# Kernel tuning notes

Hardware: AMD Instinct MI355X
Metric: run time of the kernel (lower is better)

Reference implementation:

```python
import jax, jax.numpy as jnp
import numpy as np

NHEAD = 8

def setup_inputs() -> dict:
    key = jax.random.key(0)
    ks = jax.random.split(key, 7)
    B, N, D = 8, 1024, 512
    scale = 1.0 / np.sqrt(D)
    return {
        "x": jax.random.normal(ks[0], (B, N, D), dtype=jnp.float32),
        "graph_bias": jax.random.normal(ks[1], (B, N, N), dtype=jnp.float32),
        "in_proj_w": jax.random.normal(ks[2], (3 * D, D), dtype=jnp.float32) * scale,
        "in_proj_b": jax.random.normal(ks[3], (3 * D,), dtype=jnp.float32) * 0.02,
        "out_proj_w": jax.random.normal(ks[4], (D, D), dtype=jnp.float32) * scale,
        "out_proj_b": jax.random.normal(ks[5], (D,), dtype=jnp.float32) * 0.02,
        "bias_strength": jnp.ones((), dtype=jnp.float32),
    }

def reference(x, graph_bias, in_proj_w, in_proj_b, out_proj_w, out_proj_b, bias_strength):
    B, N, D = x.shape
    H = NHEAD
    hd = D // H
    # fused QKV projection (matches nn.MultiheadAttention in_proj)
    qkv = x @ in_proj_w.T + in_proj_b          # (B, N, 3D)
    q, k, v = jnp.split(qkv, 3, axis=-1)
    # (B, H, N, hd)
    q = q.reshape(B, N, H, hd).transpose(0, 2, 1, 3)
    k = k.reshape(B, N, H, hd).transpose(0, 2, 1, 3)
    v = v.reshape(B, N, H, hd).transpose(0, 2, 1, 3)
    # additive bias from predicted causal structure
    alpha = jax.nn.sigmoid(bias_strength)
    causal_mask = jax.nn.sigmoid(graph_bias).transpose(0, 2, 1)   # (B, N, N)
    causal_mask = alpha * causal_mask + (1.0 - alpha) * 0.5
    attn_bias = (causal_mask - 0.5) * 10.0                        # (B, N, N)
    scores = jnp.einsum("bhqd,bhkd->bhqk", q, k) / jnp.sqrt(jnp.asarray(hd, x.dtype))
    scores = scores + attn_bias[:, None, :, :]                    # broadcast over heads
    probs = jax.nn.softmax(scores, axis=-1)
    out = jnp.einsum("bhqk,bhkd->bhqd", probs, v)                 # (B, H, N, hd)
    out = out.transpose(0, 2, 1, 3).reshape(B, N, D)
    return out @ out_proj_w.T + out_proj_b
```

## Files before the change

kernel.cpp:

```cpp
#include <hip/hip_runtime.h>

typedef __attribute__((ext_vector_type(8))) __bf16 bf16x8;
typedef __attribute__((ext_vector_type(4))) __bf16 bf16x4;
typedef __attribute__((ext_vector_type(4))) float f32x4;
typedef __attribute__((ext_vector_type(8))) _Float16 f16x8;

#define LOG2E 1.44269504088896340736f

__device__ __forceinline__ void async_load16(const void* g, void* l) {
  __builtin_amdgcn_global_load_lds(
      (const __attribute__((address_space(1))) void*)g,
      (__attribute__((address_space(3))) void*)l, 16, 0, 0);
}

__device__ __forceinline__ float fast_exp2(float x) {
#if __has_builtin(__builtin_amdgcn_exp2f)
  return __builtin_amdgcn_exp2f(x);
#else
  return __expf(x * 0.6931471805599453f);
#endif
}

__global__ void cvtW(const float* __restrict__ b, __bf16* __restrict__ ob, int nb4,
                     const float* __restrict__ c, __bf16* __restrict__ oc, int nc4) {
  int i = blockIdx.x * blockDim.x + threadIdx.x;
  int n = nb4 + nc4;
  int stride = gridDim.x * blockDim.x;
  for (; i < n; i += stride) {
    const float4* s;
    bf16x4* d;
    int j;
    if (i < nb4) { s = (const float4*)b; d = (bf16x4*)ob; j = i; }
    else { s = (const float4*)c; d = (bf16x4*)oc; j = i - nb4; }
    float4 v = s[j];
    bf16x4 o;
    o[0] = (__bf16)v.x; o[1] = (__bf16)v.y; o[2] = (__bf16)v.z; o[3] = (__bf16)v.w;
    d[j] = o;
  }
}

__global__ __launch_bounds__(512, 4) void gemm1_ebias(
    const float* __restrict__ X,
    const __bf16* __restrict__ Bm,
    const float* __restrict__ bias,
    __bf16* __restrict__ qkO,
    __bf16* __restrict__ vT,
    const float* __restrict__ gbias, const float* __restrict__ bstr,
    _Float16* __restrict__ ebT) {
  __shared__ __align__(16) char smem[32768];
  const int t = threadIdx.x;

  if (blockIdx.x >= 768) {
    const int gid = (blockIdx.x - 768) * 512 + t;
    const int lane = gid & 63;
    const int kt = (gid >> 6) & 31;
    const int qt = (gid >> 11) & 63;
    const int b = gid >> 17;
    const int g = lane >> 4, ln = lane & 15;
    const float alpha = 1.f / (1.f + __expf(-bstr[0]));
    const float bsc = 10.f * alpha * LOG2E;
    const float* base = gbias + (size_t)(b * 1024 + kt * 32 + ln) * 1024 + qt * 16 + g * 4;
    float4 va = *(const float4*)(base);
    float4 vb = *(const float4*)(base + 16 * 1024);
    float sv[8] = {va.x, va.y, va.z, va.w, vb.x, vb.y, vb.z, vb.w};
    f16x8 o;
#pragma unroll
    for (int i = 0; i < 8; ++i)
      o[i] = (_Float16)((1.f / (1.f + __expf(-sv[i])) - 0.5f) * bsc);
    *(f16x8*)(ebT + (size_t)gid * 8) = o;
    return;
  }

  char* lA = smem;
  char* lB = smem + 16384;
  const int lane = t & 63;
  const int wid = t >> 6;
  const int wm = wid >> 2, wn = wid & 3;
  const int g = lane >> 4, ln = lane & 15;
  const int wg = (blockIdx.x & 7) * 96 + (blockIdx.x >> 3);
  const int m0 = (wg / 12) * 128;
  const int n0 = (wg % 12) * 128;

  const int srow = t >> 3;
  const int sswz = ((t & 7) * 16) ^ ((srow & 7) << 4);
  const int eswz = ((t & 7) * 8) ^ ((srow & 7) << 3);
  const char* gB = (const char*)Bm + (size_t)n0 * 1024;
  const float* gX = X + (size_t)m0 * 512;

  f32x4 acc[4][2] = {};

  for (int k0 = 0; k0 < 512; k0 += 64) {
    __syncthreads();
#pragma unroll
    for (int c = 0; c < 2; ++c) {
      int row = srow + 64 * c;
      async_load16(gB + (size_t)row * 1024 + k0 * 2 + sswz, lB + c * 8192 + t * 16);
      const float* src = gX + (size_t)row * 512 + k0 + eswz;
      float4 a0 = *(const float4*)(src);
      float4 a1 = *(const float4*)(src + 4);
      bf16x8 o;
      o[0] = (__bf16)a0.x; o[1] = (__bf16)a0.y; o[2] = (__bf16)a0.z; o[3] = (__bf16)a0.w;
      o[4] = (__bf16)a1.x; o[5] = (__bf16)a1.y; o[6] = (__bf16)a1.z; o[7] = (__bf16)a1.w;
      *(bf16x8*)(lA + c * 8192 + t * 16) = o;
    }
    __syncthreads();
#pragma unroll
    for (int ks = 0; ks < 2; ++ks) {
      bf16x8 af[4], bf[2];
#pragma unroll
      for (int i = 0; i < 4; ++i) {
        int ar = wm * 64 + i * 16 + ln;
        af[i] = *(const bf16x8*)(lA + ar * 128 + ((ks * 64 + g * 16) ^ ((ar & 7) << 4)));
      }
#pragma unroll
      for (int j = 0; j < 2; ++j) {
        int br = wn * 32 + j * 16 + ln;
        bf[j] = *(const bf16x8*)(lB + br * 128 + ((ks * 64 + g * 16) ^ ((br & 7) << 4)));
      }
#pragma unroll
      for (int i = 0; i < 4; ++i)
#pragma unroll
        for (int j = 0; j < 2; ++j)
          acc[i][j] = __builtin_amdgcn_mfma_f32_16x16x32_bf16(af[i], bf[j], acc[i][j], 0, 0, 0);
    }
  }

#pragma unroll
  for (int j = 0; j < 2; ++j) {
    int col = n0 + wn * 32 + j * 16 + ln;
    float bv = bias[col];
    if (col < 1024) {
      float scale = (col < 512) ? (0.125f * LOG2E) : 1.0f;
#pragma unroll
      for (int i = 0; i < 4; ++i) {
        int row0 = m0 + wm * 64 + i * 16 + g * 4;
#pragma unroll
        for (int r = 0; r < 4; ++r)
          qkO[(size_t)(row0 + r) * 1024 + col] = (__bf16)((acc[i][j][r] + bv) * scale);
      }
    } else {
      int h = (col - 1024) >> 6;
      int d = (col - 1024) & 63;
#pragma unroll
      for (int i = 0; i < 4; ++i) {
        int row0 = m0 + wm * 64 + i * 16 + g * 4;
        int b = row0 >> 10;
        bf16x4 pk;
#pragma unroll
        for (int r = 0; r < 4; ++r) pk[r] = (__bf16)(acc[i][j][r] + bv);
        *(bf16x4*)(vT + (((size_t)b * 8 + h) * 64 + d) * 1024 + (row0 & 1023)) = pk;
      }
    }
  }
}

__global__ __launch_bounds__(512, 4) void gemm_bt0(
    const __bf16* __restrict__ A, const __bf16* __restrict__ Bm,
    const float* __restrict__ bias, float* __restrict__ C0,
    int M, int N, int K, int nt) {
  __shared__ __align__(16) char smem[32768];
  char* lA = smem;
  char* lB = smem + 16384;
  const int t = threadIdx.x;
  const int lane = t & 63;
  const int wid = t >> 6;
  const int wm = wid >> 2, wn = wid & 3;
  const int g = lane >> 4, ln = lane & 15;
  const int qchunk = gridDim.x >> 3;
  const int wg = (blockIdx.x & 7) * qchunk + (blockIdx.x >> 3);
  const int m0 = (wg / nt) * 128;
  const int n0 = (wg % nt) * 128;

  const int srow = t >> 3;
  const int sswz = ((t & 7) * 16) ^ ((srow & 7) << 4);
  const size_t KB = (size_t)K * 2;
  const char* gA = (const char*)A + (size_t)m0 * KB;
  const char* gB = (const char*)Bm + (size_t)n0 * KB;

  f32x4 acc[4][2] = {};

  for (int k0 = 0; k0 < K; k0 += 64) {
    __syncthreads();
#pragma unroll
    for (int c = 0; c < 2; ++c) {
      int row = srow + 64 * c;
      async_load16(gA + (size_t)row * KB + k0 * 2 + sswz, lA + c * 8192 + t * 16);
      async_load16(gB + (size_t)row * KB + k0 * 2 + sswz, lB + c * 8192 + t * 16);
    }
    __syncthreads();
#pragma unroll
    for (int ks = 0; ks < 2; ++ks) {
      bf16x8 af[4], bf[2];
#pragma unroll
      for (int i = 0; i < 4; ++i) {
        int ar = wm * 64 + i * 16 + ln;
        af[i] = *(const bf16x8*)(lA + ar * 128 + ((ks * 64 + g * 16) ^ ((ar & 7) << 4)));
      }
#pragma unroll
      for (int j = 0; j < 2; ++j) {
        int br = wn * 32 + j * 16 + ln;
        bf[j] = *(const bf16x8*)(lB + br * 128 + ((ks * 64 + g * 16) ^ ((br & 7) << 4)));
      }
#pragma unroll
      for (int i = 0; i < 4; ++i)
#pragma unroll
        for (int j = 0; j < 2; ++j)
          acc[i][j] = __builtin_amdgcn_mfma_f32_16x16x32_bf16(af[i], bf[j], acc[i][j], 0, 0, 0);
    }
  }

#pragma unroll
  for (int j = 0; j < 2; ++j) {
    int col = n0 + wn * 32 + j * 16 + ln;
    float bv = bias[col];
#pragma unroll
    for (int i = 0; i < 4; ++i) {
      int row0 = m0 + wm * 64 + i * 16 + g * 4;
#pragma unroll
      for (int r = 0; r < 4; ++r)
        C0[(size_t)(row0 + r) * N + col] = acc[i][j][r] + bv;
    }
  }
}

__global__ __launch_bounds__(512, 4) void attn_fused(
    const __bf16* __restrict__ qk,
    const __bf16* __restrict__ vT,
    const _Float16* __restrict__ ebT,
    __bf16* __restrict__ attn) {
  __shared__ __align__(16) char smem[73728];
  const int t = threadIdx.x;
  const int lane = t & 63;
  const int wid = t >> 6;
  const int g = lane >> 4, ln = lane & 15;
  const int wg = ((blockIdx.x & 7) << 6) + (blockIdx.x >> 3);
  const int b = wg >> 6;
  const int rem = wg & 63;
  const int h = rem >> 3;
  const int qg = rem & 7;
  const int qt = qg * 8 + wid;
  const int q0 = qt << 4;

  char* Ps = smem + 65536 + wid * 1024;

  bf16x8 qf[2];
#pragma unroll
  for (int ks = 0; ks < 2; ++ks)
    qf[ks] = *(const bf16x8*)(qk + ((size_t)b * 1024 + q0 + ln) * 1024 +
                              h * 64 + ks * 32 + g * 8);

  float l_acc[4] = {0.f, 0.f, 0.f, 0.f};
  f32x4 o_acc[4] = {};

  const int krow = lane >> 3;
  const int ksrc = ((lane & 7) * 16) ^ (krow << 4);
  const int vrow = lane >> 2;
  const int vsrc = ((lane & 3) * 16) ^ ((vrow & 3) << 4);

  const char* qkb = (const char*)qk + (size_t)b * 1024 * 2048;
  const char* vTb = (const char*)vT + (size_t)(b * 8 + h) * 64 * 2048;
  const _Float16* ebp = ebT + (size_t)((b * 64 + qt) * 32) * 512 + lane * 8;

  auto stage = [&](int p, char* set) {
    if (wid < 4) {
#pragma unroll
      for (int j = 0; j < 4; ++j)
        async_load16(qkb + (size_t)((4 * p + j) * 32 + wid * 8 + krow) * 2048 +
                         1024 + h * 128 + ksrc,
                     set + j * 4096 + wid * 1024 + lane * 16);
    } else {
      int cc = wid - 4;
#pragma unroll
      for (int j = 0; j < 4; ++j)
        async_load16(vTb + (size_t)(cc * 16 + vrow) * 2048 + (size_t)(4 * p + j) * 64 + vsrc,
                     set + 16384 + j * 4096 + cc * 1024 + lane * 16);
    }
  };

  auto process = [&](const char* Kp, const char* Vp, f16x8 ebv) {
    bf16x8 kf[2][2];
#pragma unroll
    for (int ni = 0; ni < 2; ++ni) {
      int br = ni * 16 + ln;
      int sw = (br & 7) << 4;
#pragma unroll
      for (int ks = 0; ks < 2; ++ks)
        kf[ni][ks] = *(const bf16x8*)(Kp + br * 128 + ((ks * 64 + g * 16) ^ sw));
    }
    bf16x8 vf[4];
#pragma unroll
    for (int di = 0; di < 4; ++di)
      vf[di] = *(const bf16x8*)(Vp + (di * 16 + ln) * 64 + ((g * 16) ^ ((ln & 3) << 4)));

    f32x4 lbf0 = {(float)ebv[0], (float)ebv[1], (float)ebv[2], (float)ebv[3]};
    f32x4 lbf1 = {(float)ebv[4], (float)ebv[5], (float)ebv[6], (float)ebv[7]};
    f32x4 s[2];
    s[0] = __builtin_amdgcn_mfma_f32_16x16x32_bf16(qf[0], kf[0][0], lbf0, 0, 0, 0);
    s[0] = __builtin_amdgcn_mfma_f32_16x16x32_bf16(qf[1], kf[0][1], s[0], 0, 0, 0);
    s[1] = __builtin_amdgcn_mfma_f32_16x16x32_bf16(qf[0], kf[1][0], lbf1, 0, 0, 0);
    s[1] = __builtin_amdgcn_mfma_f32_16x16x32_bf16(qf[1], kf[1][1], s[1], 0, 0, 0);

#pragma unroll
    for (int r = 0; r < 4; ++r) {
      float p0 = fast_exp2(s[0][r]);
      float p1 = fast_exp2(s[1][r]);
      s[0][r] = p0; s[1][r] = p1;
      l_acc[r] += p0 + p1;
    }
#pragma unroll
    for (int ni = 0; ni < 2; ++ni)
#pragma unroll
      for (int r = 0; r < 4; ++r) {
        int q = g * 4 + r;
        *(__bf16*)(Ps + q * 64 + ((ni * 32 + ln * 2) ^ (((q >> 1) & 3) << 4))) =
            (__bf16)s[ni][r];
      }
    bf16x8 pf = *(const bf16x8*)(Ps + ln * 64 + ((g * 16) ^ (((ln >> 1) & 3) << 4)));

#pragma unroll
    for (int di = 0; di < 4; ++di)
      o_acc[di] = __builtin_amdgcn_mfma_f32_16x16x32_bf16(pf, vf[di], o_acc[di], 0, 0, 0);
  };

  stage(0, smem);
  f16x8 eb0 = *(const f16x8*)(ebp);
  f16x8 eb1 = *(const f16x8*)(ebp + 512);
  f16x8 eb2 = *(const f16x8*)(ebp + 1024);
  f16x8 eb3 = *(const f16x8*)(ebp + 1536);
  asm volatile("s_waitcnt vmcnt(0)" ::: "memory");
  __syncthreads();

  for (int p = 0; p < 8; ++p) {
    char* cur = smem + (p & 1) * 32768;
    char* nxt = smem + ((p + 1) & 1) * 32768;
    const int pn = (p + 1) & 7;

    stage(pn, nxt);
    f16x8 ebn0 = *(const f16x8*)(ebp + (size_t)(4 * pn) * 512);
    f16x8 ebn1 = *(const f16x8*)(ebp + (size_t)(4 * pn + 1) * 512);
    f16x8 ebn2 = *(const f16x8*)(ebp + (size_t)(4 * pn + 2) * 512);
    f16x8 ebn3 = *(const f16x8*)(ebp + (size_t)(4 * pn + 3) * 512);
    __builtin_amdgcn_sched_barrier(0);

    process(cur,         cur + 16384, eb0);
    process(cur + 4096,  cur + 20480, eb1);
    process(cur + 8192,  cur + 24576, eb2);
    process(cur + 12288, cur + 28672, eb3);

    asm volatile("s_waitcnt vmcnt(0)" ::: "memory");
    __builtin_amdgcn_sched_barrier(0);
    __syncthreads();
    eb0 = ebn0; eb1 = ebn1; eb2 = ebn2; eb3 = ebn3;
  }

#pragma unroll
  for (int r = 0; r < 4; ++r) {
    float rs = l_acc[r];
#pragma unroll
    for (int off = 1; off < 16; off <<= 1)
      rs += __shfl_xor(rs, off, 64);
    float inv = 1.f / rs;
    int q = q0 + g * 4 + r;
#pragma unroll
    for (int di = 0; di < 4; ++di)
      attn[((size_t)b * 1024 + q) * 512 + h * 64 + di * 16 + ln] =
          (__bf16)(o_acc[di][r] * inv);
  }
}

extern "C" void kernel_launch(void* const* d_in, const int* in_sizes, int n_in,
                              void* d_out, int out_size, void* d_ws, size_t ws_size,
                              hipStream_t stream) {
  const float* x     = (const float*)d_in[0];
  const float* gb    = (const float*)d_in[1];
  const float* w_in  = (const float*)d_in[2];
  const float* b_in  = (const float*)d_in[3];
  const float* w_out = (const float*)d_in[4];
  const float* b_out = (const float*)d_in[5];
  const float* bstr  = (const float*)d_in[6];

  char* ws = (char*)d_ws;
  __bf16* qk    = (__bf16*)(ws);
  __bf16* vT    = (__bf16*)(ws + 16777216);
  __bf16* attn_buf = (__bf16*)(ws + 25165824);
  __bf16* w1    = (__bf16*)(ws + 33554432);
  __bf16* w2    = (__bf16*)(ws + 35127296);
  _Float16* ebT = (_Float16*)(ws + 35651584);

  cvtW<<<1024, 256, 0, stream>>>(w_in, w1, (1536 * 512) / 4,
                                 w_out, w2, (512 * 512) / 4);

  gemm1_ebias<<<768 + 2048, 512, 0, stream>>>(x, w1, b_in, qk, vT, gb, bstr, ebT);
  attn_fused<<<512, 512, 0, stream>>>(qk, vT, ebT, attn_buf);
  gemm_bt0<<<256, 512, 0, stream>>>(attn_buf, w2, b_out, (float*)d_out, 8192, 512, 512, 4);
}
```

Before: 81.80 us.

## Fuse graph-bias sigmoid transform into attention kernel, drop precomputed fp16 buffer

```diff
diff --git a/kernel.cpp b/kernel.cpp
--- a/kernel.cpp
+++ b/kernel.cpp
@@ -39,38 +39,14 @@
   }
 }
 
-__global__ __launch_bounds__(512, 4) void gemm1_ebias(
+__global__ __launch_bounds__(512, 4) void gemm1(
     const float* __restrict__ X,
     const __bf16* __restrict__ Bm,
     const float* __restrict__ bias,
     __bf16* __restrict__ qkO,
-    __bf16* __restrict__ vT,
-    const float* __restrict__ gbias, const float* __restrict__ bstr,
-    _Float16* __restrict__ ebT) {
+    __bf16* __restrict__ vT) {
   __shared__ __align__(16) char smem[32768];
   const int t = threadIdx.x;
-
-  if (blockIdx.x >= 768) {
-    const int gid = (blockIdx.x - 768) * 512 + t;
-    const int lane = gid & 63;
-    const int kt = (gid >> 6) & 31;
-    const int qt = (gid >> 11) & 63;
-    const int b = gid >> 17;
-    const int g = lane >> 4, ln = lane & 15;
-    const float alpha = 1.f / (1.f + __expf(-bstr[0]));
-    const float bsc = 10.f * alpha * LOG2E;
-    const float* base = gbias + (size_t)(b * 1024 + kt * 32 + ln) * 1024 + qt * 16 + g * 4;
-    float4 va = *(const float4*)(base);
-    float4 vb = *(const float4*)(base + 16 * 1024);
-    float sv[8] = {va.x, va.y, va.z, va.w, vb.x, vb.y, vb.z, vb.w};
-    f16x8 o;
-#pragma unroll
-    for (int i = 0; i < 8; ++i)
-      o[i] = (_Float16)((1.f / (1.f + __expf(-sv[i])) - 0.5f) * bsc);
-    *(f16x8*)(ebT + (size_t)gid * 8) = o;
-    return;
-  }
-
   char* lA = smem;
   char* lB = smem + 16384;
   const int lane = t & 63;
@@ -226,7 +202,8 @@
 __global__ __launch_bounds__(512, 4) void attn_fused(
     const __bf16* __restrict__ qk,
     const __bf16* __restrict__ vT,
-    const _Float16* __restrict__ ebT,
+    const float* __restrict__ gbias,
+    const float* __restrict__ bstr,
     __bf16* __restrict__ attn) {
   __shared__ __align__(16) char smem[73728];
   const int t = threadIdx.x;
@@ -243,6 +220,9 @@
 
   char* Ps = smem + 65536 + wid * 1024;
 
+  const float alpha = 1.f / (1.f + __expf(-bstr[0]));
+  const float bsc = 10.f * alpha * LOG2E;
+
   bf16x8 qf[2];
 #pragma unroll
   for (int ks = 0; ks < 2; ++ks)
@@ -259,7 +239,23 @@
 
   const char* qkb = (const char*)qk + (size_t)b * 1024 * 2048;
   const char* vTb = (const char*)vT + (size_t)(b * 8 + h) * 64 * 2048;
-  const _Float16* ebp = ebT + (size_t)((b * 64 + qt) * 32) * 512 + lane * 8;
+  const float* gbq = gbias + ((size_t)b << 20) + qt * 16 + g * 4;
+
+  auto ldrow = [&](int kt, int ni) {
+    return *(const float4*)(gbq + (size_t)(kt * 32 + ni * 16 + ln) * 1024);
+  };
+  auto sigpack = [&](float4 lo, float4 hi) {
+    f16x8 o;
+    o[0] = (_Float16)((1.f / (1.f + __expf(-lo.x)) - 0.5f) * bsc);
+    o[1] = (_Float16)((1.f / (1.f + __expf(-lo.y)) - 0.5f) * bsc);
+    o[2] = (_Float16)((1.f / (1.f + __expf(-lo.z)) - 0.5f) * bsc);
+    o[3] = (_Float16)((1.f / (1.f + __expf(-lo.w)) - 0.5f) * bsc);
+    o[4] = (_Float16)((1.f / (1.f + __expf(-hi.x)) - 0.5f) * bsc);
+    o[5] = (_Float16)((1.f / (1.f + __expf(-hi.y)) - 0.5f) * bsc);
+    o[6] = (_Float16)((1.f / (1.f + __expf(-hi.z)) - 0.5f) * bsc);
+    o[7] = (_Float16)((1.f / (1.f + __expf(-hi.w)) - 0.5f) * bsc);
+    return o;
+  };
 
   auto stage = [&](int p, char* set) {
     if (wid < 4) {
@@ -323,11 +319,15 @@
   };
 
   stage(0, smem);
-  f16x8 eb0 = *(const f16x8*)(ebp);
-  f16x8 eb1 = *(const f16x8*)(ebp + 512);
-  f16x8 eb2 = *(const f16x8*)(ebp + 1024);
-  f16x8 eb3 = *(const f16x8*)(ebp + 1536);
+  float4 bnA0 = ldrow(0, 0), bnA1 = ldrow(0, 1);
+  float4 bnB0 = ldrow(1, 0), bnB1 = ldrow(1, 1);
+  float4 bnC0 = ldrow(2, 0), bnC1 = ldrow(2, 1);
+  float4 bnD0 = ldrow(3, 0), bnD1 = ldrow(3, 1);
   asm volatile("s_waitcnt vmcnt(0)" ::: "memory");
+  f16x8 eb0 = sigpack(bnA0, bnA1);
+  f16x8 eb1 = sigpack(bnB0, bnB1);
+  f16x8 eb2 = sigpack(bnC0, bnC1);
+  f16x8 eb3 = sigpack(bnD0, bnD1);
   __syncthreads();
 
   for (int p = 0; p < 8; ++p) {
@@ -336,10 +336,10 @@
     const int pn = (p + 1) & 7;
 
     stage(pn, nxt);
-    f16x8 ebn0 = *(const f16x8*)(ebp + (size_t)(4 * pn) * 512);
-    f16x8 ebn1 = *(const f16x8*)(ebp + (size_t)(4 * pn + 1) * 512);
-    f16x8 ebn2 = *(const f16x8*)(ebp + (size_t)(4 * pn + 2) * 512);
-    f16x8 ebn3 = *(const f16x8*)(ebp + (size_t)(4 * pn + 3) * 512);
+    bnA0 = ldrow(4 * pn + 0, 0); bnA1 = ldrow(4 * pn + 0, 1);
+    bnB0 = ldrow(4 * pn + 1, 0); bnB1 = ldrow(4 * pn + 1, 1);
+    bnC0 = ldrow(4 * pn + 2, 0); bnC1 = ldrow(4 * pn + 2, 1);
+    bnD0 = ldrow(4 * pn + 3, 0); bnD1 = ldrow(4 * pn + 3, 1);
     __builtin_amdgcn_sched_barrier(0);
 
     process(cur,         cur + 16384, eb0);
@@ -350,7 +350,10 @@
     asm volatile("s_waitcnt vmcnt(0)" ::: "memory");
     __builtin_amdgcn_sched_barrier(0);
     __syncthreads();
-    eb0 = ebn0; eb1 = ebn1; eb2 = ebn2; eb3 = ebn3;
+    eb0 = sigpack(bnA0, bnA1);
+    eb1 = sigpack(bnB0, bnB1);
+    eb2 = sigpack(bnC0, bnC1);
+    eb3 = sigpack(bnD0, bnD1);
   }
 
 #pragma unroll
@@ -380,17 +383,16 @@
   const float* bstr  = (const float*)d_in[6];
 
   char* ws = (char*)d_ws;
-  __bf16* qk    = (__bf16*)(ws);
-  __bf16* vT    = (__bf16*)(ws + 16777216);
+  __bf16* qk       = (__bf16*)(ws);
+  __bf16* vT       = (__bf16*)(ws + 16777216);
   __bf16* attn_buf = (__bf16*)(ws + 25165824);
-  __bf16* w1    = (__bf16*)(ws + 33554432);
-  __bf16* w2    = (__bf16*)(ws + 35127296);
-  _Float16* ebT = (_Float16*)(ws + 35651584);
+  __bf16* w1       = (__bf16*)(ws + 33554432);
+  __bf16* w2       = (__bf16*)(ws + 35127296);
 
   cvtW<<<1024, 256, 0, stream>>>(w_in, w1, (1536 * 512) / 4,
                                  w_out, w2, (512 * 512) / 4);
 
-  gemm1_ebias<<<768 + 2048, 512, 0, stream>>>(x, w1, b_in, qk, vT, gb, bstr, ebT);
-  attn_fused<<<512, 512, 0, stream>>>(qk, vT, ebT, attn_buf);
+  gemm1<<<768, 512, 0, stream>>>(x, w1, b_in, qk, vT);
+  attn_fused<<<512, 512, 0, stream>>>(qk, vT, gb, bstr, attn_buf);
   gemm_bt0<<<256, 512, 0, stream>>>(attn_buf, w2, b_out, (float*)d_out, 8192, 512, 512, 4);
 }
```

New measurement: 144.8 us. +77.1%, slower.
